# Kernel optimization log

Measured on AMD Instinct MI355X. Metric: run time of the kernel, lower is better.

## Reference

```python
import jax, jax.numpy as jnp
import numpy as np


def setup_inputs() -> dict:
    key = jax.random.key(0)
    k1, k2, k3 = jax.random.split(key, 3)
    x = jax.random.normal(k1, (8192, 4096), dtype=jnp.float32)
    # int8 quantized weight codes (stored as int32 per harness dtypes)
    q_layer = jax.random.randint(k2, (4096, 4096), 0, 127, dtype=jnp.int32)
    weight_scale = jax.random.uniform(k3, (1,), dtype=jnp.float32)
    return {"x": x, "q_layer": q_layer, "weight_scale": weight_scale}


def reference(x, q_layer, weight_scale):
    # Dequantize: cast int codes to fp32, multiply by scalar scale.
    W_approx = q_layer.astype(jnp.float32) * weight_scale  # [out, in]
    # F.linear(x, W) = x @ W.T
    return jnp.einsum('bi,oi->bo', x, W_approx)
```

## Files before the change

kernel.cpp:

```cpp
#include <hip/hip_runtime.h>


typedef __attribute__((ext_vector_type(4))) int int4v;
typedef __attribute__((ext_vector_type(4))) float float4v;

constexpr int Mdim = 8192, Ndim = 4096, Kdim = 4096;
constexpr int BM = 256, BN = 256, BK = 64;
constexpr int NT_N = Ndim / BN;
constexpr int NWG = (Mdim / BM) * (Ndim / BN);
constexpr int NTILES = Kdim / BK;

#define GLOAD16(gp, lp)                                                      \
  __builtin_amdgcn_global_load_lds(                                          \
      (const __attribute__((address_space(1))) void*)(gp),                   \
      (__attribute__((address_space(3))) void*)(lp), 16, 0, 0)
#define FENCE() asm volatile("" ::: "memory")
#define BARRIER()                      \
  do {                                 \
    FENCE();                           \
    __builtin_amdgcn_s_barrier();      \
    FENCE();                           \
  } while (0)
#define WAIT_VM(n) asm volatile("s_waitcnt vmcnt(" #n ")" ::: "memory")

__global__ void quant_x_i8(const float* __restrict__ x,
                           signed char* __restrict__ xq,
                           float* __restrict__ sr) {
  const int row = blockIdx.x;
  const int t = threadIdx.x;
  const float4v* px = (const float4v*)(x + (size_t)row * Kdim);
  float4v v[4];
  float am = 0.f;
#pragma unroll
  for (int i = 0; i < 4; ++i) {
    v[i] = px[t * 4 + i];
#pragma unroll
    for (int j = 0; j < 4; ++j) am = fmaxf(am, fabsf(v[i][j]));
  }
#pragma unroll
  for (int off = 32; off; off >>= 1) am = fmaxf(am, __shfl_xor(am, off));
  __shared__ float wm[4];
  if ((t & 63) == 0) wm[t >> 6] = am;
  __syncthreads();
  am = fmaxf(fmaxf(wm[0], wm[1]), fmaxf(wm[2], wm[3]));
  const float rcp = am > 0.f ? 127.0f / am : 0.f;
  if (t == 0) sr[row] = am * (1.0f / 127.0f);
  int o[4];
#pragma unroll
  for (int i = 0; i < 4; ++i) {
    int q0 = __float2int_rn(v[i][0] * rcp);
    int q1 = __float2int_rn(v[i][1] * rcp);
    int q2 = __float2int_rn(v[i][2] * rcp);
    int q3 = __float2int_rn(v[i][3] * rcp);
    o[i] = (q0 & 255) | ((q1 & 255) << 8) | ((q2 & 255) << 16) | (q3 << 24);
  }
  int4v ov = {o[0], o[1], o[2], o[3]};
  ((int4v*)(xq + (size_t)row * Kdim))[t] = ov;
}

__global__ void cvt_q_i8(const int* __restrict__ q,
                         signed char* __restrict__ qq, int n16) {
  int i = blockIdx.x * blockDim.x + threadIdx.x;
  const int stride = gridDim.x * blockDim.x;
  for (; i < n16; i += stride) {
    const int4v* p = (const int4v*)q + i * 4;
    int o[4];
#pragma unroll
    for (int k = 0; k < 4; ++k) {
      int4v w = p[k];
      o[k] = w[0] | (w[1] << 8) | (w[2] << 16) | (w[3] << 24);
    }
    int4v ov = {o[0], o[1], o[2], o[3]};
    ((int4v*)qq)[i] = ov;
  }
}

__global__ __launch_bounds__(512, 2) void gemm_i8(
    const signed char* __restrict__ A, const signed char* __restrict__ B,
    float* __restrict__ C, const float* __restrict__ srow,
    const float* __restrict__ scale_p) {
  __shared__ signed char sA[4][BM * BK];
  __shared__ signed char sB[4][BN * BK];

  const int tid = threadIdx.x;
  const int wid = tid >> 6, lane = tid & 63;
  const int fr = lane & 15;
  const int kg = lane >> 4;
  const int kx = ((kg ^ ((fr >> 1) & 3)) << 4);

  const int bid = blockIdx.x;
  const int swz = (bid & 7) * (NWG / 8) + (bid >> 3);
  const int mt = swz / NT_N, ntl = swz % NT_N;
  const int brow = mt * BM, bcol = ntl * BN;

  const int wm = wid >> 2, wn = wid & 3;

  const int strow = wid * 16 + (lane >> 2);
  const int stcol = (((lane & 3) ^ ((lane >> 3) & 3)) << 4);
  const signed char* gA[2];
  const signed char* gB[2];
#pragma unroll
  for (int j = 0; j < 2; ++j) {
    gA[j] = A + (size_t)(brow + j * 128 + strow) * Kdim + stcol;
    gB[j] = B + (size_t)(bcol + j * 128 + strow) * Kdim + stcol;
  }

  auto stage4 = [&](int slot, int t) {
#pragma unroll
    for (int j = 0; j < 2; ++j)
      GLOAD16(gA[j] + t * BK, &sA[slot][j * 8192 + wid * 1024]);
#pragma unroll
    for (int j = 0; j < 2; ++j)
      GLOAD16(gB[j] + t * BK, &sB[slot][j * 8192 + wid * 1024]);
  };
  auto loadA8 = [&](int4v* af, int sl) {
#pragma unroll
    for (int ch = 0; ch < 2; ++ch)
#pragma unroll
      for (int m = 0; m < 4; ++m)
        af[ch * 4 + m] = *(const int4v*)(const void*)&sA[sl]
                             [(wm * 128 + ch * 64 + m * 16 + fr) * BK + kx];
  };
  auto loadB4 = [&](int4v* bf, int sl) {
#pragma unroll
    for (int n = 0; n < 4; ++n)
      bf[n] = *(const int4v*)(const void*)&sB[sl]
                  [(wn * 64 + n * 16 + fr) * BK + kx];
  };

  int4v acc[8][4] = {};

  auto mma32 = [&](const int4v* af, const int4v* bf) {
    __builtin_amdgcn_s_setprio(1);
#pragma unroll
    for (int ch = 0; ch < 2; ++ch)
#pragma unroll
      for (int m = 0; m < 4; ++m)
#pragma unroll
        for (int n = 0; n < 4; ++n)
          acc[ch * 4 + m][n] = __builtin_amdgcn_mfma_i32_16x16x64_i8(
              af[ch * 4 + m], bf[n], acc[ch * 4 + m][n], 0, 0, 0);
    __builtin_amdgcn_s_setprio(0);
  };

  int4v aE[8], bE[4], aO[8], bO[4];

  auto body = [&](int u, const int4v* aC, const int4v* bC, int4v* aN,
                  int4v* bN) {
    const int su1 = (u + 1) & 3;
    const int st3 = (u + 3) & 3;
    const int t3 = (u + 3 < NTILES) ? u + 3 : NTILES - 1;
    loadB4(bN, su1);
    loadA8(aN, su1);
    stage4(st3, t3);
    mma32(aC, bC);
    WAIT_VM(4);
    BARRIER();
  };

  stage4(0, 0);
  stage4(1, 1);
  stage4(2, 2);
  WAIT_VM(8);
  BARRIER();
  loadB4(bE, 0);
  loadA8(aE, 0);
  WAIT_VM(4);
  BARRIER();

#pragma unroll 2
  for (int u = 0; u < NTILES; u += 2) {
    body(u, aE, bE, aO, bO);
    body(u + 1, aO, bO, aE, bE);
  }

  WAIT_VM(0);

  const float sw = *scale_p;
  const int col0 = bcol + wn * 64 + fr;
  const int rb = (lane >> 4) * 4;
#pragma unroll
  for (int ch = 0; ch < 2; ++ch)
#pragma unroll
    for (int m = 0; m < 4; ++m)
#pragma unroll
      for (int j = 0; j < 4; ++j) {
        const int row = brow + wm * 128 + ch * 64 + m * 16 + rb + j;
        const float f = srow[row] * sw;
#pragma unroll
        for (int n = 0; n < 4; ++n)
          C[(size_t)row * Ndim + (col0 + n * 16)] =
              (float)acc[ch * 4 + m][n][j] * f;
      }
}

extern "C" void kernel_launch(void* const* d_in, const int* in_sizes, int n_in,
                              void* d_out, int out_size, void* d_ws,
                              size_t ws_size, hipStream_t stream) {
  const float* x = (const float*)d_in[0];
  const int* q = (const int*)d_in[1];
  const float* scale = (const float*)d_in[2];
  float* out = (float*)d_out;

  signed char* xq = (signed char*)d_ws;
  signed char* qq = xq + (size_t)Mdim * Kdim;
  float* sr = (float*)(qq + (size_t)Ndim * Kdim);
  const size_t ws_needed =
      (size_t)Mdim * Kdim + (size_t)Ndim * Kdim + Mdim * sizeof(float);
  if (ws_size < ws_needed) return;

  quant_x_i8<<<Mdim, 256, 0, stream>>>(x, xq, sr);
  cvt_q_i8<<<2048, 256, 0, stream>>>(q, qq, (Ndim * Kdim) / 16);
  gemm_i8<<<NWG, 512, 0, stream>>>(xq, qq, out, sr, scale);
}
```

Baseline: 192.1 us.

## Pre-tile weights in MFMA fragment order and load B directly to registers

```diff
diff --git a/kernel.cpp b/kernel.cpp
--- a/kernel.cpp
+++ b/kernel.cpp
@@ -9,6 +9,7 @@
 constexpr int NT_N = Ndim / BN;
 constexpr int NWG = (Mdim / BM) * (Ndim / BN);
 constexpr int NTILES = Kdim / BK;
+constexpr int KT = Kdim / 64;
 
 #define GLOAD16(gp, lp)                                                      \
   __builtin_amdgcn_global_load_lds(                                          \
@@ -39,10 +40,10 @@
   }
 #pragma unroll
   for (int off = 32; off; off >>= 1) am = fmaxf(am, __shfl_xor(am, off));
-  __shared__ float wm[4];
-  if ((t & 63) == 0) wm[t >> 6] = am;
+  __shared__ float wmx[4];
+  if ((t & 63) == 0) wmx[t >> 6] = am;
   __syncthreads();
-  am = fmaxf(fmaxf(wm[0], wm[1]), fmaxf(wm[2], wm[3]));
+  am = fmaxf(fmaxf(wmx[0], wmx[1]), fmaxf(wmx[2], wmx[3]));
   const float rcp = am > 0.f ? 127.0f / am : 0.f;
   if (t == 0) sr[row] = am * (1.0f / 127.0f);
   int o[4];
@@ -58,29 +59,28 @@
   ((int4v*)(xq + (size_t)row * Kdim))[t] = ov;
 }
 
-__global__ void cvt_q_i8(const int* __restrict__ q,
-                         signed char* __restrict__ qq, int n16) {
-  int i = blockIdx.x * blockDim.x + threadIdx.x;
-  const int stride = gridDim.x * blockDim.x;
-  for (; i < n16; i += stride) {
-    const int4v* p = (const int4v*)q + i * 4;
-    int o[4];
-#pragma unroll
-    for (int k = 0; k < 4; ++k) {
-      int4v w = p[k];
-      o[k] = w[0] | (w[1] << 8) | (w[2] << 16) | (w[3] << 24);
-    }
-    int4v ov = {o[0], o[1], o[2], o[3]};
-    ((int4v*)qq)[i] = ov;
-  }
+__global__ void cvt_q_i8_tiled(const int* __restrict__ q,
+                               signed char* __restrict__ qq) {
+  const int tile = blockIdx.x * 4 + (threadIdx.x >> 6);
+  const int lane = threadIdx.x & 63;
+  const int n = (tile / KT) * 16 + (lane & 15);
+  const int k0 = (tile % KT) * 64 + (lane >> 4) * 16;
+  const int4v* src = (const int4v*)(q + (size_t)n * Kdim + k0);
+  int o[4];
+#pragma unroll
+  for (int i = 0; i < 4; ++i) {
+    int4v w = src[i];
+    o[i] = w[0] | (w[1] << 8) | (w[2] << 16) | (w[3] << 24);
+  }
+  int4v ov = {o[0], o[1], o[2], o[3]};
+  ((int4v*)qq)[(size_t)tile * 64 + lane] = ov;
 }
 
 __global__ __launch_bounds__(512, 2) void gemm_i8(
-    const signed char* __restrict__ A, const signed char* __restrict__ B,
+    const signed char* __restrict__ A, const signed char* __restrict__ Bt,
     float* __restrict__ C, const float* __restrict__ srow,
     const float* __restrict__ scale_p) {
   __shared__ signed char sA[4][BM * BK];
-  __shared__ signed char sB[4][BN * BK];
 
   const int tid = threadIdx.x;
   const int wid = tid >> 6, lane = tid & 63;
@@ -98,34 +98,27 @@
   const int strow = wid * 16 + (lane >> 2);
   const int stcol = (((lane & 3) ^ ((lane >> 3) & 3)) << 4);
   const signed char* gA[2];
-  const signed char* gB[2];
-#pragma unroll
-  for (int j = 0; j < 2; ++j) {
+#pragma unroll
+  for (int j = 0; j < 2; ++j)
     gA[j] = A + (size_t)(brow + j * 128 + strow) * Kdim + stcol;
-    gB[j] = B + (size_t)(bcol + j * 128 + strow) * Kdim + stcol;
-  }
-
-  auto stage4 = [&](int slot, int t) {
+
+  auto stageA2 = [&](int slot, int t) {
 #pragma unroll
     for (int j = 0; j < 2; ++j)
       GLOAD16(gA[j] + t * BK, &sA[slot][j * 8192 + wid * 1024]);
-#pragma unroll
-    for (int j = 0; j < 2; ++j)
-      GLOAD16(gB[j] + t * BK, &sB[slot][j * 8192 + wid * 1024]);
   };
   auto loadA8 = [&](int4v* af, int sl) {
 #pragma unroll
-    for (int ch = 0; ch < 2; ++ch)
-#pragma unroll
-      for (int m = 0; m < 4; ++m)
-        af[ch * 4 + m] = *(const int4v*)(const void*)&sA[sl]
-                             [(wm * 128 + ch * 64 + m * 16 + fr) * BK + kx];
-  };
-  auto loadB4 = [&](int4v* bf, int sl) {
+    for (int i = 0; i < 8; ++i)
+      af[i] = *(const int4v*)(const void*)&sA[sl]
+                  [(wm * 128 + i * 16 + fr) * BK + kx];
+  };
+  const int4v* Bw4 =
+      (const int4v*)Bt + ((size_t)(bcol / 16) + wn * 4) * KT * 64 + lane;
+  auto loadB4g = [&](int4v* bf, int t) {
 #pragma unroll
     for (int n = 0; n < 4; ++n)
-      bf[n] = *(const int4v*)(const void*)&sB[sl]
-                  [(wn * 64 + n * 16 + fr) * BK + kx];
+      bf[n] = Bw4[((size_t)n * KT + t) * 64];
   };
 
   int4v acc[8][4] = {};
@@ -133,13 +126,11 @@
   auto mma32 = [&](const int4v* af, const int4v* bf) {
     __builtin_amdgcn_s_setprio(1);
 #pragma unroll
-    for (int ch = 0; ch < 2; ++ch)
-#pragma unroll
-      for (int m = 0; m < 4; ++m)
-#pragma unroll
-        for (int n = 0; n < 4; ++n)
-          acc[ch * 4 + m][n] = __builtin_amdgcn_mfma_i32_16x16x64_i8(
-              af[ch * 4 + m], bf[n], acc[ch * 4 + m][n], 0, 0, 0);
+    for (int i = 0; i < 8; ++i)
+#pragma unroll
+      for (int n = 0; n < 4; ++n)
+        acc[i][n] = __builtin_amdgcn_mfma_i32_16x16x64_i8(
+            af[i], bf[n], acc[i][n], 0, 0, 0);
     __builtin_amdgcn_s_setprio(0);
   };
 
@@ -147,28 +138,26 @@
 
   auto body = [&](int u, const int4v* aC, const int4v* bC, int4v* aN,
                   int4v* bN) {
-    const int su1 = (u + 1) & 3;
-    const int st3 = (u + 3) & 3;
+    const int sn = (u + 1) & 3;
+    const int tB = (u + 1 < NTILES) ? u + 1 : NTILES - 1;
+    const int st = (u + 3) & 3;
     const int t3 = (u + 3 < NTILES) ? u + 3 : NTILES - 1;
-    loadB4(bN, su1);
-    loadA8(aN, su1);
-    stage4(st3, t3);
+    loadB4g(bN, tB);
+    loadA8(aN, sn);
+    stageA2(st, t3);
     mma32(aC, bC);
-    WAIT_VM(4);
+    WAIT_VM(2);
     BARRIER();
   };
 
-  stage4(0, 0);
-  stage4(1, 1);
-  stage4(2, 2);
-  WAIT_VM(8);
-  BARRIER();
-  loadB4(bE, 0);
-  loadA8(aE, 0);
+  stageA2(0, 0);
+  stageA2(1, 1);
+  stageA2(2, 2);
+  loadB4g(bE, 0);
   WAIT_VM(4);
   BARRIER();
-
-#pragma unroll 2
+  loadA8(aE, 0);
+
   for (int u = 0; u < NTILES; u += 2) {
     body(u, aE, bE, aO, bO);
     body(u + 1, aO, bO, aE, bE);
@@ -180,18 +169,15 @@
   const int col0 = bcol + wn * 64 + fr;
   const int rb = (lane >> 4) * 4;
 #pragma unroll
-  for (int ch = 0; ch < 2; ++ch)
-#pragma unroll
-    for (int m = 0; m < 4; ++m)
-#pragma unroll
-      for (int j = 0; j < 4; ++j) {
-        const int row = brow + wm * 128 + ch * 64 + m * 16 + rb + j;
-        const float f = srow[row] * sw;
-#pragma unroll
-        for (int n = 0; n < 4; ++n)
-          C[(size_t)row * Ndim + (col0 + n * 16)] =
-              (float)acc[ch * 4 + m][n][j] * f;
-      }
+  for (int i = 0; i < 8; ++i)
+#pragma unroll
+    for (int j = 0; j < 4; ++j) {
+      const int row = brow + wm * 128 + i * 16 + rb + j;
+      const float f = srow[row] * sw;
+#pragma unroll
+      for (int n = 0; n < 4; ++n)
+        C[(size_t)row * Ndim + (col0 + n * 16)] = (float)acc[i][n][j] * f;
+    }
 }
 
 extern "C" void kernel_launch(void* const* d_in, const int* in_sizes, int n_in,
@@ -210,6 +196,6 @@
   if (ws_size < ws_needed) return;
 
   quant_x_i8<<<Mdim, 256, 0, stream>>>(x, xq, sr);
-  cvt_q_i8<<<2048, 256, 0, stream>>>(q, qq, (Ndim * Kdim) / 16);
+  cvt_q_i8_tiled<<<4096, 256, 0, stream>>>(q, qq);
   gemm_i8<<<NWG, 512, 0, stream>>>(xq, qq, out, sr, scale);
 }
```

After: 189.6 us. Within noise of the previous version (-1.3%).
